# Optimization experiments

Measured on AMD Instinct MI355X. Metric: run time of the kernel, lower is better.

Reference implementation:

```python
import jax, jax.numpy as jnp
import numpy as np

B, T, D = 2, 4096, 768
H = 12
DK = D // H


def setup_inputs() -> dict:
    key = jax.random.key(0)
    k1, k2, k3 = jax.random.split(key, 3)
    x = jax.random.normal(k1, (B, T, D), dtype=jnp.float32)
    W_qkv = jax.random.normal(k2, (D, 3 * D), dtype=jnp.float32) * (1.0 / np.sqrt(D))
    b_qkv = jnp.zeros((3 * D,), dtype=jnp.float32)
    W_proj = jax.random.normal(k3, (D, D), dtype=jnp.float32) * (1.0 / np.sqrt(D))
    b_proj = jnp.zeros((D,), dtype=jnp.float32)
    return {"x": x, "W_qkv": W_qkv, "b_qkv": b_qkv, "W_proj": W_proj, "b_proj": b_proj}


def reference(x, W_qkv, b_qkv, W_proj, b_proj):
    b, t, c = x.shape
    qkv = x @ W_qkv + b_qkv                      # [B,T,3D]
    q, k, v = jnp.split(qkv, 3, axis=-1)
    q = q.reshape(b, t, H, DK)                   # [B,T,H,DK]
    k = k.reshape(b, t, H, DK)
    v = v.reshape(b, t, H, DK)
    scale = 1.0 / np.sqrt(DK)
    scores = jnp.einsum('bthd,bshd->bhts', q, k) * scale   # [B,H,T,T]
    causal = jnp.tril(jnp.ones((t, t), dtype=bool))
    scores = jnp.where(causal[None, None], scores, jnp.float32(-jnp.inf))
    probs = jax.nn.softmax(scores, axis=-1)      # dropout p=0.0 -> identity
    out = jnp.einsum('bhts,bshd->bthd', probs, v).reshape(b, t, c)
    return out @ W_proj + b_proj
```

## Files before the change

### kernel.cpp

```cpp
#include <hip/hip_runtime.h>
#include <hip/hip_bf16.h>
#include <cstdint>
#include <cstddef>


typedef __attribute__((ext_vector_type(8))) short bf16x8;
typedef __attribute__((ext_vector_type(4))) short bf16x4;
typedef __attribute__((ext_vector_type(4))) float f32x4;

#define MFMA16(a, b, c)   __builtin_amdgcn_mfma_f32_16x16x32_bf16((a), (b), (c), 0, 0, 0)
#define MFMA16K(a, b, c)  __builtin_amdgcn_mfma_f32_16x16x16bf16_1k((a), (b), (c), 0, 0, 0)

static constexpr int Bc = 2, Tc = 4096, Dc = 768, Hc = 12, DKc = 64;
static constexpr int BHc = Bc * Hc;
static constexpr int Mc = Bc * Tc;
static constexpr int Nqkv = 3 * Dc;
static constexpr int NQBLK = Tc / 128;
static constexpr unsigned int NITEMS = BHc * NQBLK;

__device__ __forceinline__ unsigned short f2bf(float f) {
    union { float f; unsigned int i; } c; c.f = f;
    unsigned int x = c.i;
    return (unsigned short)((x + 0x7fffu + ((x >> 16) & 1u)) >> 16);
}
__device__ __forceinline__ unsigned int pkbf(float a, float b) {
    __hip_bfloat162 h = __float22bfloat162_rn(make_float2(a, b));
    union { __hip_bfloat162 h; unsigned int u; } c; c.h = h;
    return c.u;
}
__device__ __forceinline__ void glds16(const unsigned short* g, unsigned short* l) {
    __builtin_amdgcn_global_load_lds(
        (const __attribute__((address_space(1))) unsigned int*)g,
        (__attribute__((address_space(3))) unsigned int*)l, 16, 0, 0);
}

__global__ __launch_bounds__(256)
void xconv_kernel(const float* __restrict__ X, unsigned short* __restrict__ Xb) {
    size_t i = ((size_t)blockIdx.x * 256 + threadIdx.x) * 8;
    float4 a = *(const float4*)(X + i);
    float4 b = *(const float4*)(X + i + 4);
    uint4 o;
    o.x = pkbf(a.x, a.y); o.y = pkbf(a.z, a.w);
    o.z = pkbf(b.x, b.y); o.w = pkbf(b.z, b.w);
    *(uint4*)(Xb + i) = o;
}

__global__ __launch_bounds__(256)
void wtrans_kernel(const float* __restrict__ W, unsigned short* __restrict__ WT,
                   int K, int N) {
    __shared__ __align__(16) unsigned short tile[64 * 72];
    const int k0 = blockIdx.x * 64;
    const int n0 = blockIdx.y * 64;
    const int tid = threadIdx.x;
#pragma unroll
    for (int it = 0; it < 4; ++it) {
        int s = tid + it * 256;
        int r = s >> 4, g = s & 15;
        float4 v = *(const float4*)(W + (size_t)(k0 + r) * N + n0 + g * 4);
        ushort4 u;
        u.x = f2bf(v.x); u.y = f2bf(v.y); u.z = f2bf(v.z); u.w = f2bf(v.w);
        *(ushort4*)(tile + r * 72 + g * 4) = u;
    }
    __syncthreads();
#pragma unroll
    for (int it = 0; it < 2; ++it) {
        int s = tid + it * 256;
        int n = s >> 3, g = s & 7;
        unsigned int p0 = (unsigned int)tile[(g * 8 + 0) * 72 + n] |
                          ((unsigned int)tile[(g * 8 + 1) * 72 + n] << 16);
        unsigned int p1 = (unsigned int)tile[(g * 8 + 2) * 72 + n] |
                          ((unsigned int)tile[(g * 8 + 3) * 72 + n] << 16);
        unsigned int p2 = (unsigned int)tile[(g * 8 + 4) * 72 + n] |
                          ((unsigned int)tile[(g * 8 + 5) * 72 + n] << 16);
        unsigned int p3 = (unsigned int)tile[(g * 8 + 6) * 72 + n] |
                          ((unsigned int)tile[(g * 8 + 7) * 72 + n] << 16);
        uint4 o; o.x = p0; o.y = p1; o.z = p2; o.w = p3;
        *(uint4*)(WT + (size_t)(n0 + n) * K + k0 + g * 8) = o;
    }
}

__global__ __launch_bounds__(256)
void qkv_gemm_kernel(const unsigned short* __restrict__ Xb,
                     const unsigned short* __restrict__ WT,
                     const float* __restrict__ bias,
                     unsigned short* __restrict__ Qb, unsigned short* __restrict__ Kb,
                     unsigned short* __restrict__ Vt) {
    __shared__ __align__(16) unsigned short As[128 * 64];
    __shared__ __align__(16) unsigned short Bs[128 * 64];
    const int tid = threadIdx.x;
    const int wave = tid >> 6, lane = tid & 63;
    const int quad = lane >> 4, l15 = lane & 15;
    const int wr = wave >> 1, wc = wave & 1;
    const int r0 = blockIdx.x * 128, c0 = blockIdx.y * 128;
    const int sw = l15 & 7;

    f32x4 acc[4][4];
#pragma unroll
    for (int i = 0; i < 4; ++i)
#pragma unroll
        for (int j = 0; j < 4; ++j) acc[i][j] = (f32x4){0.f, 0.f, 0.f, 0.f};

    for (int k0 = 0; k0 < Dc; k0 += 64) {
#pragma unroll
        for (int it = 0; it < 4; ++it) {
            int idx = it * 256 + tid;
            int r = idx >> 3, c = idx & 7;
            int cg = c ^ (r & 7);
            glds16(Xb + (size_t)(r0 + r) * Dc + k0 + cg * 8, As + idx * 8);
            glds16(WT + (size_t)(c0 + r) * Dc + k0 + cg * 8, Bs + idx * 8);
        }
        __syncthreads();
#pragma unroll
        for (int f = 0; f < 2; ++f) {
            bf16x8 af[4], bfr[4];
#pragma unroll
            for (int mt = 0; mt < 4; ++mt)
                af[mt] = *(const bf16x8*)(As + (wr * 64 + mt * 16 + l15) * 64 +
                                          (((f * 4 + quad) ^ sw) * 8));
#pragma unroll
            for (int nt = 0; nt < 4; ++nt)
                bfr[nt] = *(const bf16x8*)(Bs + (wc * 64 + nt * 16 + l15) * 64 +
                                           (((f * 4 + quad) ^ sw) * 8));
#pragma unroll
            for (int mt = 0; mt < 4; ++mt)
#pragma unroll
                for (int nt = 0; nt < 4; ++nt)
                    acc[mt][nt] = MFMA16(af[mt], bfr[nt], acc[mt][nt]);
        }
        __syncthreads();
    }

    const int part = c0 / Dc;
    const int cbase = c0 - part * Dc;
    const float scale = (part == 0) ? 0.125f * 1.4426950408889634f : 1.0f;
    float bv[4];
#pragma unroll
    for (int nt = 0; nt < 4; ++nt) bv[nt] = bias[c0 + wc * 64 + nt * 16 + l15];

    if (part < 2) {
        unsigned short* dstbuf = (part == 0) ? Qb : Kb;
#pragma unroll
        for (int mt = 0; mt < 4; ++mt)
#pragma unroll
            for (int reg = 0; reg < 4; ++reg) {
                int gr = r0 + wr * 64 + mt * 16 + quad * 4 + reg;
                int b = gr >> 12, t = gr & 4095;
#pragma unroll
                for (int nt = 0; nt < 4; ++nt) {
                    int cc = cbase + wc * 64 + nt * 16 + l15;
                    int h = cc >> 6, dk = cc & 63;
                    float v = (acc[mt][nt][reg] + bv[nt]) * scale;
                    dstbuf[((size_t)(b * Hc + h) * Tc + t) * DKc + dk] = f2bf(v);
                }
            }
    } else {
#pragma unroll
        for (int mt = 0; mt < 4; ++mt)
#pragma unroll
            for (int reg = 0; reg < 4; ++reg) {
                int gr = r0 + wr * 64 + mt * 16 + quad * 4 + reg;
                int b = gr >> 12, t = gr & 4095;
#pragma unroll
                for (int nt = 0; nt < 4; ++nt) {
                    int cc = cbase + wc * 64 + nt * 16 + l15;
                    int h = cc >> 6, dk = cc & 63;
                    float v = acc[mt][nt][reg] + bv[nt];
                    Vt[((size_t)(b * Hc + h) * DKc + dk) * Tc + t] = f2bf(v);
                }
            }
    }
}

__global__ __launch_bounds__(256)
void attn_kernel(const unsigned short* __restrict__ Qb,
                 const unsigned short* __restrict__ Kb,
                 const unsigned short* __restrict__ Vt,
                 unsigned short* __restrict__ attn,
                 unsigned int* __restrict__ counter) {
    __shared__ __align__(16) unsigned short Ks[64 * 64];
    __shared__ __align__(16) unsigned short Vs[64 * 64];
    __shared__ unsigned int s_w;
    const int tid = threadIdx.x;
    const int wave = tid >> 6, lane = tid & 63;
    const int quad = lane >> 4, l15 = lane & 15;
    const int sw = l15 & 7;

    for (;;) {
        if (tid == 0) s_w = atomicAdd(counter, 1u);
        __syncthreads();
        const unsigned int w = s_w;
        if (w >= NITEMS) break;
        const int bh = (int)(w % (unsigned)BHc);
        const int i0 = (NQBLK - 1 - (int)(w / (unsigned)BHc)) * 128;
        const unsigned short* Qp = Qb + (size_t)bh * Tc * DKc;
        const unsigned short* Kp = Kb + (size_t)bh * Tc * DKc;
        const unsigned short* Vp = Vt + (size_t)bh * DKc * Tc;

        bf16x8 qf[2][2];
#pragma unroll
        for (int qg = 0; qg < 2; ++qg)
#pragma unroll
            for (int f = 0; f < 2; ++f)
                qf[qg][f] = *(const bf16x8*)(Qp +
                    (size_t)(i0 + wave * 32 + qg * 16 + l15) * DKc + f * 32 + quad * 8);

        f32x4 lp[2] = {(f32x4){0.f,0.f,0.f,0.f}, (f32x4){0.f,0.f,0.f,0.f}};
        f32x4 o[2][4];
#pragma unroll
        for (int qg = 0; qg < 2; ++qg)
#pragma unroll
            for (int d = 0; d < 4; ++d) o[qg][d] = (f32x4){0.f, 0.f, 0.f, 0.f};

        const int jmax = (i0 >> 6) + 1;
        for (int jt = 0; jt <= jmax; ++jt) {
            const int j0 = jt * 64;
#pragma unroll
            for (int it = 0; it < 2; ++it) {
                int idx = it * 256 + tid;
                int r = idx >> 3, c = idx & 7;
                int cg = c ^ (r & 7);
                glds16(Kp + (size_t)(j0 + r) * DKc + cg * 8, Ks + idx * 8);
                glds16(Vp + (size_t)r * Tc + j0 + cg * 8, Vs + idx * 8);
            }
            __syncthreads();

            bf16x8 kf[2][4];
            bf16x4 vf[4][4];
#pragma unroll
            for (int f = 0; f < 2; ++f)
#pragma unroll
                for (int mt = 0; mt < 4; ++mt)
                    kf[f][mt] = *(const bf16x8*)(Ks + (mt * 16 + l15) * 64 +
                                                 (((f * 4 + quad) ^ sw) * 8));
#pragma unroll
            for (int d = 0; d < 4; ++d)
#pragma unroll
                for (int mt = 0; mt < 4; ++mt) {
                    int g8 = mt * 4 + quad;
                    vf[d][mt] = *(const bf16x4*)(Vs + (d * 16 + l15) * 64 +
                                                 (((g8 >> 1) ^ sw) * 8) + (g8 & 1) * 4);
                }
            __syncthreads();

            f32x4 sc[2][4];
#pragma unroll
            for (int qg = 0; qg < 2; ++qg)
#pragma unroll
                for (int mt = 0; mt < 4; ++mt) sc[qg][mt] = (f32x4){0.f, 0.f, 0.f, 0.f};
#pragma unroll
            for (int f = 0; f < 2; ++f)
#pragma unroll
                for (int mt = 0; mt < 4; ++mt) {
                    sc[0][mt] = MFMA16(kf[f][mt], qf[0][f], sc[0][mt]);
                    sc[1][mt] = MFMA16(kf[f][mt], qf[1][f], sc[1][mt]);
                }

            const int rel = j0 - i0;
            if (jt >= jmax - 1) {
#pragma unroll
                for (int qg = 0; qg < 2; ++qg) {
                    int qrow = wave * 32 + qg * 16 + l15;
#pragma unroll
                    for (int mt = 0; mt < 4; ++mt)
#pragma unroll
                        for (int reg = 0; reg < 4; ++reg)
                            if (rel + mt * 16 + quad * 4 + reg > qrow)
                                sc[qg][mt][reg] = -1e30f;
                }
            }

            union { uint2 u; bf16x4 v; } pb[2][4];
#pragma unroll
            for (int qg = 0; qg < 2; ++qg)
#pragma unroll
                for (int mt = 0; mt < 4; ++mt) {
#pragma unroll
                    for (int reg = 0; reg < 4; ++reg)
                        sc[qg][mt][reg] = __builtin_amdgcn_exp2f(sc[qg][mt][reg]);
                    lp[qg] += sc[qg][mt];
                    pb[qg][mt].u.x = pkbf(sc[qg][mt][0], sc[qg][mt][1]);
                    pb[qg][mt].u.y = pkbf(sc[qg][mt][2], sc[qg][mt][3]);
                }

#pragma unroll
            for (int mt = 0; mt < 4; ++mt)
#pragma unroll
                for (int d = 0; d < 4; ++d) {
                    o[0][d] = MFMA16K(vf[d][mt], pb[0][mt].v, o[0][d]);
                    o[1][d] = MFMA16K(vf[d][mt], pb[1][mt].v, o[1][d]);
                }
        }

        const int b = bh / Hc, h = bh % Hc;
#pragma unroll
        for (int qg = 0; qg < 2; ++qg) {
            float ls = lp[qg][0] + lp[qg][1] + lp[qg][2] + lp[qg][3];
            ls += __shfl_xor(ls, 16);
            ls += __shfl_xor(ls, 32);
            float li = 1.0f / ls;
            int t = i0 + wave * 32 + qg * 16 + l15;
            unsigned short* dst = attn + (size_t)(b * Tc + t) * Dc + h * 64;
#pragma unroll
            for (int d = 0; d < 4; ++d) {
                uint2 u;
                u.x = pkbf(o[qg][d][0] * li, o[qg][d][1] * li);
                u.y = pkbf(o[qg][d][2] * li, o[qg][d][3] * li);
                *(uint2*)(dst + d * 16 + quad * 4) = u;
            }
        }
    }
}

__global__ __launch_bounds__(256)
void proj_gemm_kernel(const unsigned short* __restrict__ A,
                      const unsigned short* __restrict__ WT,
                      const float* __restrict__ bias, float* __restrict__ out) {
    __shared__ __align__(16) unsigned short As[128 * 64];
    __shared__ __align__(16) unsigned short Bs[128 * 64];
    const int tid = threadIdx.x;
    const int wave = tid >> 6, lane = tid & 63;
    const int quad = lane >> 4, l15 = lane & 15;
    const int wr = wave >> 1, wc = wave & 1;
    const int r0 = blockIdx.x * 128, c0 = blockIdx.y * 128;
    const int sw = l15 & 7;

    f32x4 acc[4][4];
#pragma unroll
    for (int i = 0; i < 4; ++i)
#pragma unroll
        for (int j = 0; j < 4; ++j) acc[i][j] = (f32x4){0.f, 0.f, 0.f, 0.f};

    for (int k0 = 0; k0 < Dc; k0 += 64) {
#pragma unroll
        for (int it = 0; it < 4; ++it) {
            int idx = it * 256 + tid;
            int r = idx >> 3, c = idx & 7;
            int cg = c ^ (r & 7);
            glds16(A + (size_t)(r0 + r) * Dc + k0 + cg * 8, As + idx * 8);
            glds16(WT + (size_t)(c0 + r) * Dc + k0 + cg * 8, Bs + idx * 8);
        }
        __syncthreads();
#pragma unroll
        for (int f = 0; f < 2; ++f) {
            bf16x8 af[4], bfr[4];
#pragma unroll
            for (int mt = 0; mt < 4; ++mt)
                af[mt] = *(const bf16x8*)(As + (wr * 64 + mt * 16 + l15) * 64 +
                                          (((f * 4 + quad) ^ sw) * 8));
#pragma unroll
            for (int nt = 0; nt < 4; ++nt)
                bfr[nt] = *(const bf16x8*)(Bs + (wc * 64 + nt * 16 + l15) * 64 +
                                           (((f * 4 + quad) ^ sw) * 8));
#pragma unroll
            for (int mt = 0; mt < 4; ++mt)
#pragma unroll
                for (int nt = 0; nt < 4; ++nt)
                    acc[mt][nt] = MFMA16(af[mt], bfr[nt], acc[mt][nt]);
        }
        __syncthreads();
    }

    float bv[4];
#pragma unroll
    for (int nt = 0; nt < 4; ++nt) bv[nt] = bias[c0 + wc * 64 + nt * 16 + l15];
#pragma unroll
    for (int mt = 0; mt < 4; ++mt)
#pragma unroll
        for (int reg = 0; reg < 4; ++reg) {
            int gr = r0 + wr * 64 + mt * 16 + quad * 4 + reg;
#pragma unroll
            for (int nt = 0; nt < 4; ++nt) {
                int gc = c0 + wc * 64 + nt * 16 + l15;
                out[(size_t)gr * Dc + gc] = acc[mt][nt][reg] + bv[nt];
            }
        }
}

extern "C" void kernel_launch(void* const* d_in, const int* in_sizes, int n_in,
                              void* d_out, int out_size, void* d_ws, size_t ws_size,
                              hipStream_t stream) {
    const float* x      = (const float*)d_in[0];
    const float* W_qkv  = (const float*)d_in[1];
    const float* b_qkv  = (const float*)d_in[2];
    const float* W_proj = (const float*)d_in[3];
    const float* b_proj = (const float*)d_in[4];
    float* out = (float*)d_out;

    char* ws = (char*)d_ws;
    size_t off = 0;
    auto take = [&](size_t bytes) -> char* {
        char* p = ws + off;
        off += (bytes + 255) & ~(size_t)255;
        return p;
    };
    unsigned int*   cnt = (unsigned int*)take(256);
    unsigned short* WqT = (unsigned short*)take((size_t)Nqkv * Dc * 2);
    unsigned short* WpT = (unsigned short*)take((size_t)Dc * Dc * 2);
    unsigned short* Qb  = (unsigned short*)take((size_t)BHc * Tc * DKc * 2);
    unsigned short* Kb  = (unsigned short*)take((size_t)BHc * Tc * DKc * 2);
    unsigned short* Vt  = (unsigned short*)take((size_t)BHc * Tc * DKc * 2);
    unsigned short* Xb  = (unsigned short*)take((size_t)Mc * Dc * 2);
    unsigned short* An  = Xb;

    hipMemsetAsync(cnt, 0, sizeof(unsigned int), stream);
    xconv_kernel<<<dim3((Mc * Dc) / (256 * 8)), dim3(256), 0, stream>>>(x, Xb);
    wtrans_kernel<<<dim3(Dc / 64, Nqkv / 64), dim3(256), 0, stream>>>(W_qkv, WqT, Dc, Nqkv);
    wtrans_kernel<<<dim3(Dc / 64, Dc / 64), dim3(256), 0, stream>>>(W_proj, WpT, Dc, Dc);
    qkv_gemm_kernel<<<dim3(Mc / 128, Nqkv / 128), dim3(256), 0, stream>>>(Xb, WqT, b_qkv, Qb, Kb, Vt);
    attn_kernel<<<dim3(NITEMS), dim3(256), 0, stream>>>(Qb, Kb, Vt, An, cnt);
    proj_gemm_kernel<<<dim3(Mc / 128, Dc / 128), dim3(256), 0, stream>>>(An, WpT, b_proj, out);
}
```

Before: 258.2 us.

## Double-buffer K/V tiles in attention with async prefetch and MFMA priority hints

The attention loop now keeps two shared-memory buffers for K and V. It issues the global-to-LDS loads for the next key tile before computing on the current one, using explicit vmcnt waits and raw barriers in place of __syncthreads. This overlaps memory latency with the MFMA and exp work. It also raises wave priority around the MFMA blocks with s_setprio. The cost is twice the LDS footprint, which may reduce occupancy, and the hand-written waitcnt values must match the number of outstanding loads.

Result: slower. 270.4 us (+4.7%).

```diff
diff --git a/kernel.cpp b/kernel.cpp
--- a/kernel.cpp
+++ b/kernel.cpp
@@ -177,8 +177,8 @@
                  const unsigned short* __restrict__ Vt,
                  unsigned short* __restrict__ attn,
                  unsigned int* __restrict__ counter) {
-    __shared__ __align__(16) unsigned short Ks[64 * 64];
-    __shared__ __align__(16) unsigned short Vs[64 * 64];
+    __shared__ __align__(16) unsigned short Ks[2][64 * 64];
+    __shared__ __align__(16) unsigned short Vs[2][64 * 64];
     __shared__ unsigned int s_w;
     const int tid = threadIdx.x;
     const int wave = tid >> 6, lane = tid & 63;
@@ -211,42 +211,58 @@
 #pragma unroll
             for (int d = 0; d < 4; ++d) o[qg][d] = (f32x4){0.f, 0.f, 0.f, 0.f};
 
-        const int jmax = (i0 >> 6) + 1;
-        for (int jt = 0; jt <= jmax; ++jt) {
+        auto stage = [&](int buf, int jt) {
             const int j0 = jt * 64;
 #pragma unroll
             for (int it = 0; it < 2; ++it) {
                 int idx = it * 256 + tid;
                 int r = idx >> 3, c = idx & 7;
                 int cg = c ^ (r & 7);
-                glds16(Kp + (size_t)(j0 + r) * DKc + cg * 8, Ks + idx * 8);
-                glds16(Vp + (size_t)r * Tc + j0 + cg * 8, Vs + idx * 8);
-            }
-            __syncthreads();
-
+                glds16(Kp + (size_t)(j0 + r) * DKc + cg * 8, &Ks[buf][idx * 8]);
+                glds16(Vp + (size_t)r * Tc + j0 + cg * 8, &Vs[buf][idx * 8]);
+            }
+        };
+
+        const int jmax = (i0 >> 6) + 1;
+        stage(0, 0);
+        int cur = 0;
+        for (int jt = 0; jt <= jmax; ++jt) {
+            const int j0 = jt * 64;
+            if (jt < jmax) {
+                stage(cur ^ 1, jt + 1);
+                asm volatile("s_waitcnt vmcnt(4)" ::: "memory");
+            } else {
+                asm volatile("s_waitcnt vmcnt(0)" ::: "memory");
+            }
+            __builtin_amdgcn_s_barrier();
+
+            const unsigned short* Kc = Ks[cur];
+            const unsigned short* Vc = Vs[cur];
             bf16x8 kf[2][4];
             bf16x4 vf[4][4];
 #pragma unroll
             for (int f = 0; f < 2; ++f)
 #pragma unroll
                 for (int mt = 0; mt < 4; ++mt)
-                    kf[f][mt] = *(const bf16x8*)(Ks + (mt * 16 + l15) * 64 +
+                    kf[f][mt] = *(const bf16x8*)(Kc + (mt * 16 + l15) * 64 +
                                                  (((f * 4 + quad) ^ sw) * 8));
 #pragma unroll
             for (int d = 0; d < 4; ++d)
 #pragma unroll
                 for (int mt = 0; mt < 4; ++mt) {
                     int g8 = mt * 4 + quad;
-                    vf[d][mt] = *(const bf16x4*)(Vs + (d * 16 + l15) * 64 +
+                    vf[d][mt] = *(const bf16x4*)(Vc + (d * 16 + l15) * 64 +
                                                  (((g8 >> 1) ^ sw) * 8) + (g8 & 1) * 4);
                 }
-            __syncthreads();
+            asm volatile("s_waitcnt lgkmcnt(0)" ::: "memory");
+            __builtin_amdgcn_s_barrier();
 
             f32x4 sc[2][4];
 #pragma unroll
             for (int qg = 0; qg < 2; ++qg)
 #pragma unroll
                 for (int mt = 0; mt < 4; ++mt) sc[qg][mt] = (f32x4){0.f, 0.f, 0.f, 0.f};
+            __builtin_amdgcn_s_setprio(1);
 #pragma unroll
             for (int f = 0; f < 2; ++f)
 #pragma unroll
@@ -254,6 +270,7 @@
                     sc[0][mt] = MFMA16(kf[f][mt], qf[0][f], sc[0][mt]);
                     sc[1][mt] = MFMA16(kf[f][mt], qf[1][f], sc[1][mt]);
                 }
+            __builtin_amdgcn_s_setprio(0);
 
             const int rel = j0 - i0;
             if (jt >= jmax - 1) {
@@ -282,6 +299,7 @@
                     pb[qg][mt].u.y = pkbf(sc[qg][mt][2], sc[qg][mt][3]);
                 }
 
+            __builtin_amdgcn_s_setprio(1);
 #pragma unroll
             for (int mt = 0; mt < 4; ++mt)
 #pragma unroll
@@ -289,6 +307,8 @@
                     o[0][d] = MFMA16K(vf[d][mt], pb[0][mt].v, o[0][d]);
                     o[1][d] = MFMA16K(vf[d][mt], pb[1][mt].v, o[1][d]);
                 }
+            __builtin_amdgcn_s_setprio(0);
+            cur ^= 1;
         }
 
         const int b = bh / Hc, h = bh % Hc;
```

## Load 128-key K/V tiles per barrier and add MFMA priority hints

Applied to the files above, without the earlier changes.

The attention inner loop now stages 128 keys of K and V per iteration instead of 64, processing them as two 64-key halves, which halves the number of global-to-LDS load rounds and block barriers. The second barrier is moved to just after the second half's LDS fragment reads, and s_setprio is raised around the MFMA sections to favour matrix issue. The causal mask is applied only on the last 128-wide tile. In exchange, LDS usage doubles and fully masked 64-key sub-tiles on the diagonal are now computed.

Result: slower. 310.0 us (+20.1%).

```diff
diff --git a/kernel.cpp b/kernel.cpp
--- a/kernel.cpp
+++ b/kernel.cpp
@@ -177,8 +177,8 @@
                  const unsigned short* __restrict__ Vt,
                  unsigned short* __restrict__ attn,
                  unsigned int* __restrict__ counter) {
-    __shared__ __align__(16) unsigned short Ks[64 * 64];
-    __shared__ __align__(16) unsigned short Vs[64 * 64];
+    __shared__ __align__(16) unsigned short Ks[128 * 64];
+    __shared__ __align__(16) unsigned short Vs[64 * 128];
     __shared__ unsigned int s_w;
     const int tid = threadIdx.x;
     const int wave = tid >> 6, lane = tid & 63;
@@ -211,84 +211,94 @@
 #pragma unroll
             for (int d = 0; d < 4; ++d) o[qg][d] = (f32x4){0.f, 0.f, 0.f, 0.f};
 
-        const int jmax = (i0 >> 6) + 1;
-        for (int jt = 0; jt <= jmax; ++jt) {
-            const int j0 = jt * 64;
-#pragma unroll
-            for (int it = 0; it < 2; ++it) {
+        const int nbig = (i0 >> 7) + 1;
+        for (int jt = 0; jt < nbig; ++jt) {
+            const int j0 = jt * 128;
+#pragma unroll
+            for (int it = 0; it < 4; ++it) {
                 int idx = it * 256 + tid;
-                int r = idx >> 3, c = idx & 7;
-                int cg = c ^ (r & 7);
-                glds16(Kp + (size_t)(j0 + r) * DKc + cg * 8, Ks + idx * 8);
-                glds16(Vp + (size_t)r * Tc + j0 + cg * 8, Vs + idx * 8);
+                int rk = idx >> 3, ck = idx & 7;
+                glds16(Kp + (size_t)(j0 + rk) * DKc + ((ck ^ (rk & 7)) * 8), Ks + idx * 8);
+                int rv = idx >> 4, cv = idx & 15;
+                glds16(Vp + (size_t)rv * Tc + j0 + ((cv ^ (rv & 7)) * 8), Vs + idx * 8);
             }
             __syncthreads();
 
-            bf16x8 kf[2][4];
-            bf16x4 vf[4][4];
-#pragma unroll
-            for (int f = 0; f < 2; ++f)
+            const bool last = (jt == nbig - 1);
+#pragma unroll
+            for (int h = 0; h < 2; ++h) {
+                bf16x8 kf[2][4];
+                bf16x4 vf[4][4];
+#pragma unroll
+                for (int f = 0; f < 2; ++f)
+#pragma unroll
+                    for (int mt = 0; mt < 4; ++mt)
+                        kf[f][mt] = *(const bf16x8*)(Ks + (h * 64 + mt * 16 + l15) * 64 +
+                                                     (((f * 4 + quad) ^ sw) * 8));
+#pragma unroll
+                for (int d = 0; d < 4; ++d)
+#pragma unroll
+                    for (int mt = 0; mt < 4; ++mt) {
+                        int g8 = h * 8 + mt * 2 + (quad >> 1);
+                        vf[d][mt] = *(const bf16x4*)(Vs + (d * 16 + l15) * 128 +
+                                                     ((g8 ^ sw) * 8) + (quad & 1) * 4);
+                    }
+                if (h == 1) {
+                    asm volatile("s_waitcnt lgkmcnt(0)" ::: "memory");
+                    __builtin_amdgcn_s_barrier();
+                }
+
+                f32x4 sc[2][4];
+#pragma unroll
+                for (int qg = 0; qg < 2; ++qg)
+#pragma unroll
+                    for (int mt = 0; mt < 4; ++mt) sc[qg][mt] = (f32x4){0.f, 0.f, 0.f, 0.f};
+                __builtin_amdgcn_s_setprio(1);
+#pragma unroll
+                for (int f = 0; f < 2; ++f)
+#pragma unroll
+                    for (int mt = 0; mt < 4; ++mt) {
+                        sc[0][mt] = MFMA16(kf[f][mt], qf[0][f], sc[0][mt]);
+                        sc[1][mt] = MFMA16(kf[f][mt], qf[1][f], sc[1][mt]);
+                    }
+                __builtin_amdgcn_s_setprio(0);
+
+                if (last) {
+#pragma unroll
+                    for (int qg = 0; qg < 2; ++qg) {
+                        int qrow = wave * 32 + qg * 16 + l15;
+#pragma unroll
+                        for (int mt = 0; mt < 4; ++mt)
+#pragma unroll
+                            for (int reg = 0; reg < 4; ++reg)
+                                if (h * 64 + mt * 16 + quad * 4 + reg > qrow)
+                                    sc[qg][mt][reg] = -1e30f;
+                    }
+                }
+
+                union { uint2 u; bf16x4 v; } pb[2][4];
+#pragma unroll
+                for (int qg = 0; qg < 2; ++qg)
+#pragma unroll
+                    for (int mt = 0; mt < 4; ++mt) {
+#pragma unroll
+                        for (int reg = 0; reg < 4; ++reg)
+                            sc[qg][mt][reg] = __builtin_amdgcn_exp2f(sc[qg][mt][reg]);
+                        lp[qg] += sc[qg][mt];
+                        pb[qg][mt].u.x = pkbf(sc[qg][mt][0], sc[qg][mt][1]);
+                        pb[qg][mt].u.y = pkbf(sc[qg][mt][2], sc[qg][mt][3]);
+                    }
+
+                __builtin_amdgcn_s_setprio(1);
 #pragma unroll
                 for (int mt = 0; mt < 4; ++mt)
-                    kf[f][mt] = *(const bf16x8*)(Ks + (mt * 16 + l15) * 64 +
-                                                 (((f * 4 + quad) ^ sw) * 8));
-#pragma unroll
-            for (int d = 0; d < 4; ++d)
-#pragma unroll
-                for (int mt = 0; mt < 4; ++mt) {
-                    int g8 = mt * 4 + quad;
-                    vf[d][mt] = *(const bf16x4*)(Vs + (d * 16 + l15) * 64 +
-                                                 (((g8 >> 1) ^ sw) * 8) + (g8 & 1) * 4);
-                }
-            __syncthreads();
-
-            f32x4 sc[2][4];
-#pragma unroll
-            for (int qg = 0; qg < 2; ++qg)
-#pragma unroll
-                for (int mt = 0; mt < 4; ++mt) sc[qg][mt] = (f32x4){0.f, 0.f, 0.f, 0.f};
-#pragma unroll
-            for (int f = 0; f < 2; ++f)
-#pragma unroll
-                for (int mt = 0; mt < 4; ++mt) {
-                    sc[0][mt] = MFMA16(kf[f][mt], qf[0][f], sc[0][mt]);
-                    sc[1][mt] = MFMA16(kf[f][mt], qf[1][f], sc[1][mt]);
-                }
-
-            const int rel = j0 - i0;
-            if (jt >= jmax - 1) {
-#pragma unroll
-                for (int qg = 0; qg < 2; ++qg) {
-                    int qrow = wave * 32 + qg * 16 + l15;
-#pragma unroll
-                    for (int mt = 0; mt < 4; ++mt)
-#pragma unroll
-                        for (int reg = 0; reg < 4; ++reg)
-                            if (rel + mt * 16 + quad * 4 + reg > qrow)
-                                sc[qg][mt][reg] = -1e30f;
-                }
-            }
-
-            union { uint2 u; bf16x4 v; } pb[2][4];
-#pragma unroll
-            for (int qg = 0; qg < 2; ++qg)
-#pragma unroll
-                for (int mt = 0; mt < 4; ++mt) {
-#pragma unroll
-                    for (int reg = 0; reg < 4; ++reg)
-                        sc[qg][mt][reg] = __builtin_amdgcn_exp2f(sc[qg][mt][reg]);
-                    lp[qg] += sc[qg][mt];
-                    pb[qg][mt].u.x = pkbf(sc[qg][mt][0], sc[qg][mt][1]);
-                    pb[qg][mt].u.y = pkbf(sc[qg][mt][2], sc[qg][mt][3]);
-                }
-
-#pragma unroll
-            for (int mt = 0; mt < 4; ++mt)
-#pragma unroll
-                for (int d = 0; d < 4; ++d) {
-                    o[0][d] = MFMA16K(vf[d][mt], pb[0][mt].v, o[0][d]);
-                    o[1][d] = MFMA16K(vf[d][mt], pb[1][mt].v, o[1][d]);
-                }
+#pragma unroll
+                    for (int d = 0; d < 4; ++d) {
+                        o[0][d] = MFMA16K(vf[d][mt], pb[0][mt].v, o[0][d]);
+                        o[1][d] = MFMA16K(vf[d][mt], pb[1][mt].v, o[1][d]);
+                    }
+                __builtin_amdgcn_s_setprio(0);
+            }
         }
 
         const int b = bh / Hc, h = bh % Hc;
```

## Shrink attention query tile to 64 rows and raise MFMA priority

Applied to the files above, without the earlier changes.

Each attention work item now covers 64 query rows instead of 128, one 16-row group per wave. This doubles the number of work items for finer causal load balancing, and the diagonal masking now hits only the last key tile. The trailing LDS barrier is replaced by an explicit lgkmcnt wait plus s_barrier, and the MFMA sections are wrapped in s_setprio. The cost is that each K/V tile loaded into LDS now feeds half as many query rows, so K/V traffic per output roughly doubles.

Result: slower. 271.0 us (+5.0%).

```diff
diff --git a/kernel.cpp b/kernel.cpp
--- a/kernel.cpp
+++ b/kernel.cpp
@@ -15,8 +15,8 @@
 static constexpr int BHc = Bc * Hc;
 static constexpr int Mc = Bc * Tc;
 static constexpr int Nqkv = 3 * Dc;
-static constexpr int NQBLK = Tc / 128;
-static constexpr unsigned int NITEMS = BHc * NQBLK;
+static constexpr int NQB64 = Tc / 64;
+static constexpr unsigned int NITEMS = BHc * NQB64;
 
 __device__ __forceinline__ unsigned short f2bf(float f) {
     union { float f; unsigned int i; } c; c.f = f;
@@ -184,6 +184,7 @@
     const int wave = tid >> 6, lane = tid & 63;
     const int quad = lane >> 4, l15 = lane & 15;
     const int sw = l15 & 7;
+    const f32x4 czero = (f32x4){0.f, 0.f, 0.f, 0.f};
 
     for (;;) {
         if (tid == 0) s_w = atomicAdd(counter, 1u);
@@ -191,27 +192,23 @@
         const unsigned int w = s_w;
         if (w >= NITEMS) break;
         const int bh = (int)(w % (unsigned)BHc);
-        const int i0 = (NQBLK - 1 - (int)(w / (unsigned)BHc)) * 128;
+        const int i0 = (NQB64 - 1 - (int)(w / (unsigned)BHc)) * 64;
         const unsigned short* Qp = Qb + (size_t)bh * Tc * DKc;
         const unsigned short* Kp = Kb + (size_t)bh * Tc * DKc;
         const unsigned short* Vp = Vt + (size_t)bh * DKc * Tc;
 
-        bf16x8 qf[2][2];
-#pragma unroll
-        for (int qg = 0; qg < 2; ++qg)
-#pragma unroll
-            for (int f = 0; f < 2; ++f)
-                qf[qg][f] = *(const bf16x8*)(Qp +
-                    (size_t)(i0 + wave * 32 + qg * 16 + l15) * DKc + f * 32 + quad * 8);
-
-        f32x4 lp[2] = {(f32x4){0.f,0.f,0.f,0.f}, (f32x4){0.f,0.f,0.f,0.f}};
-        f32x4 o[2][4];
-#pragma unroll
-        for (int qg = 0; qg < 2; ++qg)
-#pragma unroll
-            for (int d = 0; d < 4; ++d) o[qg][d] = (f32x4){0.f, 0.f, 0.f, 0.f};
-
-        const int jmax = (i0 >> 6) + 1;
+        bf16x8 qf[2];
+#pragma unroll
+        for (int f = 0; f < 2; ++f)
+            qf[f] = *(const bf16x8*)(Qp +
+                (size_t)(i0 + wave * 16 + l15) * DKc + f * 32 + quad * 8);
+
+        f32x4 lp = (f32x4){0.f, 0.f, 0.f, 0.f};
+        f32x4 o[4];
+#pragma unroll
+        for (int d = 0; d < 4; ++d) o[d] = (f32x4){0.f, 0.f, 0.f, 0.f};
+
+        const int jmax = i0 >> 6;
         for (int jt = 0; jt <= jmax; ++jt) {
             const int j0 = jt * 64;
 #pragma unroll
@@ -240,73 +237,61 @@
                     vf[d][mt] = *(const bf16x4*)(Vs + (d * 16 + l15) * 64 +
                                                  (((g8 >> 1) ^ sw) * 8) + (g8 & 1) * 4);
                 }
-            __syncthreads();
-
-            f32x4 sc[2][4];
-#pragma unroll
-            for (int qg = 0; qg < 2; ++qg)
-#pragma unroll
-                for (int mt = 0; mt < 4; ++mt) sc[qg][mt] = (f32x4){0.f, 0.f, 0.f, 0.f};
-#pragma unroll
-            for (int f = 0; f < 2; ++f)
-#pragma unroll
-                for (int mt = 0; mt < 4; ++mt) {
-                    sc[0][mt] = MFMA16(kf[f][mt], qf[0][f], sc[0][mt]);
-                    sc[1][mt] = MFMA16(kf[f][mt], qf[1][f], sc[1][mt]);
-                }
-
-            const int rel = j0 - i0;
-            if (jt >= jmax - 1) {
-#pragma unroll
-                for (int qg = 0; qg < 2; ++qg) {
-                    int qrow = wave * 32 + qg * 16 + l15;
-#pragma unroll
-                    for (int mt = 0; mt < 4; ++mt)
-#pragma unroll
-                        for (int reg = 0; reg < 4; ++reg)
-                            if (rel + mt * 16 + quad * 4 + reg > qrow)
-                                sc[qg][mt][reg] = -1e30f;
-                }
-            }
-
-            union { uint2 u; bf16x4 v; } pb[2][4];
-#pragma unroll
-            for (int qg = 0; qg < 2; ++qg)
-#pragma unroll
-                for (int mt = 0; mt < 4; ++mt) {
+            asm volatile("s_waitcnt lgkmcnt(0)" ::: "memory");
+            __builtin_amdgcn_s_barrier();
+
+            f32x4 sc[4];
+            __builtin_amdgcn_s_setprio(1);
+#pragma unroll
+            for (int mt = 0; mt < 4; ++mt) {
+                sc[mt] = MFMA16(kf[0][mt], qf[0], czero);
+                sc[mt] = MFMA16(kf[1][mt], qf[1], sc[mt]);
+            }
+            __builtin_amdgcn_s_setprio(0);
+
+            if (jt == jmax) {
+                int qrow = wave * 16 + l15;
+#pragma unroll
+                for (int mt = 0; mt < 4; ++mt)
 #pragma unroll
                     for (int reg = 0; reg < 4; ++reg)
-                        sc[qg][mt][reg] = __builtin_amdgcn_exp2f(sc[qg][mt][reg]);
-                    lp[qg] += sc[qg][mt];
-                    pb[qg][mt].u.x = pkbf(sc[qg][mt][0], sc[qg][mt][1]);
-                    pb[qg][mt].u.y = pkbf(sc[qg][mt][2], sc[qg][mt][3]);
-                }
-
-#pragma unroll
-            for (int mt = 0; mt < 4; ++mt)
-#pragma unroll
-                for (int d = 0; d < 4; ++d) {
-                    o[0][d] = MFMA16K(vf[d][mt], pb[0][mt].v, o[0][d]);
-                    o[1][d] = MFMA16K(vf[d][mt], pb[1][mt].v, o[1][d]);
-                }
+                        if (mt * 16 + quad * 4 + reg > qrow)
+                            sc[mt][reg] = -1e30f;
+            }
+
+            union { uint2 u; bf16x4 v; } pb[4];
+#pragma unroll
+            for (int mt = 0; mt < 4; ++mt) {
+#pragma unroll
+                for (int reg = 0; reg < 4; ++reg)
+                    sc[mt][reg] = __builtin_amdgcn_exp2f(sc[mt][reg]);
+                lp += sc[mt];
+                pb[mt].u.x = pkbf(sc[mt][0], sc[mt][1]);
+                pb[mt].u.y = pkbf(sc[mt][2], sc[mt][3]);
+            }
+
+            __builtin_amdgcn_s_setprio(1);
+#pragma unroll
+            for (int mt = 0; mt < 4; ++mt)
+#pragma unroll
+                for (int d = 0; d < 4; ++d)
+                    o[d] = MFMA16K(vf[d][mt], pb[mt].v, o[d]);
+            __builtin_amdgcn_s_setprio(0);
         }
 
         const int b = bh / Hc, h = bh % Hc;
-#pragma unroll
-        for (int qg = 0; qg < 2; ++qg) {
-            float ls = lp[qg][0] + lp[qg][1] + lp[qg][2] + lp[qg][3];
-            ls += __shfl_xor(ls, 16);
-            ls += __shfl_xor(ls, 32);
-            float li = 1.0f / ls;
-            int t = i0 + wave * 32 + qg * 16 + l15;
-            unsigned short* dst = attn + (size_t)(b * Tc + t) * Dc + h * 64;
-#pragma unroll
-            for (int d = 0; d < 4; ++d) {
-                uint2 u;
-                u.x = pkbf(o[qg][d][0] * li, o[qg][d][1] * li);
-                u.y = pkbf(o[qg][d][2] * li, o[qg][d][3] * li);
-                *(uint2*)(dst + d * 16 + quad * 4) = u;
-            }
+        float ls = lp[0] + lp[1] + lp[2] + lp[3];
+        ls += __shfl_xor(ls, 16);
+        ls += __shfl_xor(ls, 32);
+        float li = 1.0f / ls;
+        int t = i0 + wave * 16 + l15;
+        unsigned short* dst = attn + (size_t)(b * Tc + t) * Dc + h * 64;
+#pragma unroll
+        for (int d = 0; d < 4; ++d) {
+            uint2 u;
+            u.x = pkbf(o[d][0] * li, o[d][1] * li);
+            u.y = pkbf(o[d][2] * li, o[d][3] * li);
+            *(uint2*)(dst + d * 16 + quad * 4) = u;
         }
     }
 }
```
